# Kernel optimization log

Hardware: AMD Instinct MI355X
Metric: run time of the kernel (lower is better)

The kernel has to match this reference:

```python
import jax, jax.numpy as jnp
import numpy as np

N, S, E, HEADS = 8, 2048, 1024, 16


def setup_inputs() -> dict:
    root = jax.random.key(0)
    k1, k2, k3, k4, k5, k6 = jax.random.split(root, 6)
    query = jax.random.normal(k1, (N, S, E), jnp.float32)
    key_t = jax.random.normal(k2, (N, S, E), jnp.float32)
    value = jax.random.normal(k3, (N, S, E), jnp.float32)
    # mask broadcasts against the (buggy) energy tensor of shape (N, S, H, H)
    mask = jax.random.randint(k4, (1, 1, HEADS, HEADS), 0, 2, jnp.int32)
    # guarantee no all-masked softmax row (avoid NaN)
    diag = jnp.arange(HEADS)
    mask = mask.at[0, 0, diag, diag].set(1)
    W_out = jax.random.normal(k5, (E, E), jnp.float32) / np.float32(np.sqrt(E))
    b_out = jax.random.normal(k6, (E,), jnp.float32) * 0.02
    return {"query": query, "key": key_t, "value": value, "mask": mask,
            "W_out": W_out, "b_out": b_out, "heads": HEADS}


def reference(query, key, value, mask, W_out, b_out, heads):
    # Faithful translation of the original forward, INCLUDING its einsum-label
    # bug: tensors are transposed to (N, H, S, D) but the einsum subscripts
    # treat axis 1 as 'q/k' and axis 2 as 'h', so softmax runs over heads.
    n, q_len, e = query.shape
    d = e // heads
    inv_scale = np.float32(1.0 / np.sqrt(d))
    q = query.reshape(n, q_len, heads, d).transpose(0, 2, 1, 3)   # (N,H,S,D)
    k = key.reshape(n, q_len, heads, d).transpose(0, 2, 1, 3)     # (N,H,S,D)
    v = value.reshape(n, q_len, heads, d).transpose(0, 2, 1, 3)   # (N,H,S,D)
    # labels applied to transposed tensors -> energy shape (N, S, H, H)
    energy = jnp.einsum('nqhd,nkhd->nhqk', q, k) * inv_scale
    energy = jnp.where(mask == 0, -jnp.inf, energy)
    attention = jax.nn.softmax(energy, axis=-1)                   # over heads axis
    out = jnp.einsum('nhql,nlhd->nqhd', attention, v)             # (N,H,S,D)
    out = out.reshape(n, q_len, e)                                # raw memory reinterp, as torch does
    return out @ W_out.T + b_out
```

## Files before the change

### kernel.cpp

```cpp
#include <hip/hip_runtime.h>
#include <stdint.h>

#define S_LEN 2048
#define EMB 1024

typedef __bf16 bf16x8 __attribute__((ext_vector_type(8)));
typedef __bf16 bf16x4 __attribute__((ext_vector_type(4)));
typedef float f32x4 __attribute__((ext_vector_type(4)));

__device__ __forceinline__ unsigned short f2bf(float f) {
  unsigned int b = __float_as_uint(f);
  b += 0x7FFFu + ((b >> 16) & 1u);
  return (unsigned short)(b >> 16);
}

__device__ __forceinline__ bf16x8 cvt8(float4 a, float4 b) {
  bf16x8 r;
  r[0] = (__bf16)a.x; r[1] = (__bf16)a.y; r[2] = (__bf16)a.z; r[3] = (__bf16)a.w;
  r[4] = (__bf16)b.x; r[5] = (__bf16)b.y; r[6] = (__bf16)b.z; r[7] = (__bf16)b.w;
  return r;
}

#define GLD16(gp, lp)                                                          \
  __builtin_amdgcn_global_load_lds(                                            \
      (const __attribute__((address_space(1))) void*)(gp),                     \
      (__attribute__((address_space(3))) void*)(lp), 16, 0, 0)

__global__ __launch_bounds__(256) void attn_kernel(
    const float* __restrict__ Q, const float* __restrict__ K,
    const float* __restrict__ V, const int* __restrict__ mask,
    __bf16* __restrict__ X) {
  __shared__ __bf16 As[4][16][16];

  const int lane = threadIdx.x & 63;
  const int wv = threadIdx.x >> 6;
  const int pos = blockIdx.x * 4 + wv;
  const int n = pos >> 11;
  const int s = pos & 2047;
  const int col = lane & 15;
  const int grp = lane >> 4;
  const int gc = grp & 1;

  const float* qrow = Q + (size_t)pos * EMB;
  const float* krow = K + (size_t)pos * EMB;
  const float* vrow = V + (size_t)pos * EMB;

  const int fo = col * 64 + grp * 8;
  bf16x8 qa[2], kb[2];
#pragma unroll
  for (int t = 0; t < 2; ++t) {
    float4 a0 = *(const float4*)(qrow + fo + t * 32);
    float4 a1 = *(const float4*)(qrow + fo + t * 32 + 4);
    float4 b0 = *(const float4*)(krow + fo + t * 32);
    float4 b1 = *(const float4*)(krow + fo + t * 32 + 4);
    qa[t] = cvt8(a0, a1);
    kb[t] = cvt8(b0, b1);
  }

  f32x4 en = {0.f, 0.f, 0.f, 0.f};
  en = __builtin_amdgcn_mfma_f32_16x16x32_bf16(kb[0], qa[0], en, 0, 0, 0);
  en = __builtin_amdgcn_mfma_f32_16x16x32_bf16(kb[1], qa[1], en, 0, 0, 0);

  const int4 mrow = *(const int4*)(mask + col * 16 + grp * 4);
  float p[4];
  p[0] = (mrow.x == 0) ? -1e30f : en[0] * 0.125f;
  p[1] = (mrow.y == 0) ? -1e30f : en[1] * 0.125f;
  p[2] = (mrow.z == 0) ? -1e30f : en[2] * 0.125f;
  p[3] = (mrow.w == 0) ? -1e30f : en[3] * 0.125f;
  float mx = fmaxf(fmaxf(p[0], p[1]), fmaxf(p[2], p[3]));
  mx = fmaxf(mx, __shfl_xor(mx, 16));
  mx = fmaxf(mx, __shfl_xor(mx, 32));
  float ex[4], sm = 0.f;
#pragma unroll
  for (int r = 0; r < 4; ++r) {
    ex[r] = __expf(p[r] - mx);
    sm += ex[r];
  }
  sm += __shfl_xor(sm, 16);
  sm += __shfl_xor(sm, 32);
  const float inv = __builtin_amdgcn_rcpf(sm);

  bf16x4 aw;
#pragma unroll
  for (int r = 0; r < 4; ++r) aw[r] = (__bf16)(ex[r] * inv);
  *(bf16x4*)&As[wv][col][grp * 4] = aw;

  const bf16x8 pt = *(const bf16x8*)&As[wv][col][gc * 8];
  bf16x8 pa;
#pragma unroll
  for (int e = 0; e < 8; ++e) pa[e] = (grp < 2) ? pt[e] : (__bf16)0.f;

  const size_t xrow = (size_t)n * S_LEN + (size_t)col * 128 + (s >> 4);
  __bf16* xp = X + xrow * EMB + (size_t)((s & 15) * 64 + grp * 4);
#pragma unroll
  for (int c = 0; c < 4; ++c) {
    bf16x8 vf;
#pragma unroll
    for (int e = 0; e < 8; ++e)
      vf[e] = (__bf16)vrow[(gc * 8 + e) * 64 + c * 16 + col];
    f32x4 o = {0.f, 0.f, 0.f, 0.f};
    o = __builtin_amdgcn_mfma_f32_16x16x32_bf16(vf, pa, o, 0, 0, 0);
    bf16x4 w;
#pragma unroll
    for (int r = 0; r < 4; ++r) w[r] = (__bf16)o[r];
    *(bf16x4*)(xp + c * 16) = w;
  }
}

__global__ __launch_bounds__(256) void wconv_kernel(
    const float* __restrict__ W, unsigned short* __restrict__ Wb) {
  const int idx = blockIdx.x * 256 + threadIdx.x;
  float4 w = *(const float4*)(W + (size_t)idx * 4);
  ushort4 o;
  o.x = f2bf(w.x);
  o.y = f2bf(w.y);
  o.z = f2bf(w.z);
  o.w = f2bf(w.w);
  *(ushort4*)(Wb + (size_t)idx * 4) = o;
}

__global__ __launch_bounds__(256) void gemm_kernel(
    const unsigned short* __restrict__ A, const unsigned short* __restrict__ B,
    const float* __restrict__ bias, float* __restrict__ C) {
  __shared__ unsigned short sA[128 * 32];
  __shared__ unsigned short sB[128 * 32];

  int bid = blockIdx.x;
  const int cpx = gridDim.x >> 3;
  bid = (bid & 7) * cpx + (bid >> 3);
  const int tileM = (bid >> 3) * 128;
  const int tileN = (bid & 7) * 128;

  const int t = threadIdx.x;
  const int lane = t & 63;
  const int wid = t >> 6;
  const int wm = wid >> 1, wn = wid & 1;
  const int lrow = lane & 15;
  const int lgrp = lane >> 4;

  f32x4 acc[4][4];
#pragma unroll
  for (int a = 0; a < 4; ++a)
#pragma unroll
    for (int b = 0; b < 4; ++b) acc[a][b] = (f32x4){0.f, 0.f, 0.f, 0.f};

  const int row0 = t >> 2;
  const int kk = (t & 3) * 8;
  const size_t abase = ((size_t)(tileM + row0)) * 1024 + kk;
  const size_t bbase = ((size_t)(tileN + row0)) * 1024 + kk;

  for (int k0 = 0; k0 < 1024; k0 += 32) {
#pragma unroll
    for (int c = 0; c < 2; ++c) {
      GLD16(A + abase + (size_t)c * 64 * 1024 + k0,
            (char*)sA + c * 4096 + t * 16);
      GLD16(B + bbase + (size_t)c * 64 * 1024 + k0,
            (char*)sB + c * 4096 + t * 16);
    }
    __syncthreads();

    bf16x8 af[4], bfr[4];
#pragma unroll
    for (int mi = 0; mi < 4; ++mi)
      af[mi] = *(const bf16x8*)&sA[(wm * 64 + mi * 16 + lrow) * 32 + lgrp * 8];
#pragma unroll
    for (int ni = 0; ni < 4; ++ni)
      bfr[ni] = *(const bf16x8*)&sB[(wn * 64 + ni * 16 + lrow) * 32 + lgrp * 8];
#pragma unroll
    for (int mi = 0; mi < 4; ++mi)
#pragma unroll
      for (int ni = 0; ni < 4; ++ni)
        acc[mi][ni] = __builtin_amdgcn_mfma_f32_16x16x32_bf16(
            af[mi], bfr[ni], acc[mi][ni], 0, 0, 0);
    __syncthreads();
  }

#pragma unroll
  for (int ni = 0; ni < 4; ++ni) {
    const int colc = tileN + wn * 64 + ni * 16 + lrow;
    const float bv = bias[colc];
#pragma unroll
    for (int mi = 0; mi < 4; ++mi) {
      const int row = tileM + wm * 64 + mi * 16 + lgrp * 4;
#pragma unroll
      for (int r = 0; r < 4; ++r)
        C[(size_t)(row + r) * 1024 + colc] = acc[mi][ni][r] + bv;
    }
  }
}

extern "C" void kernel_launch(void* const* d_in, const int* in_sizes, int n_in,
                              void* d_out, int out_size, void* d_ws,
                              size_t ws_size, hipStream_t stream) {
  const float* Q = (const float*)d_in[0];
  const float* K = (const float*)d_in[1];
  const float* V = (const float*)d_in[2];
  const int* mask = (const int*)d_in[3];
  const float* W = (const float*)d_in[4];
  const float* bias = (const float*)d_in[5];
  float* out = (float*)d_out;

  __bf16* X = (__bf16*)d_ws;
  unsigned short* Wb =
      (unsigned short*)((char*)d_ws + (size_t)32 * 1024 * 1024);

  hipLaunchKernelGGL(attn_kernel, dim3(8 * S_LEN / 4), dim3(256), 0, stream, Q,
                     K, V, mask, X);
  hipLaunchKernelGGL(wconv_kernel, dim3(1024), dim3(256), 0, stream, W, Wb);
  hipLaunchKernelGGL(gemm_kernel, dim3(1024), dim3(256), 0, stream,
                     (const unsigned short*)X, Wb, bias, out);
}
```

Before: 100.7 us.

## Stage Q/K/V rows through LDS with swizzle and coalesce attention output stores

The attention kernel now loads each block's four Q, K and V rows into shared memory using direct global-to-LDS 16-byte loads, with an XOR swizzle on Q/K to avoid bank conflicts. Fragments are then read from LDS instead of through strided global gathers, especially for V, which was previously read element by element. Outputs are staged in an LDS buffer and written as contiguous 16-element bf16 vectors instead of scattered 4-element stores. This costs about 48KB of LDS per block plus extra barriers, which may limit occupancy.

```diff
diff --git a/kernel.cpp b/kernel.cpp
--- a/kernel.cpp
+++ b/kernel.cpp
@@ -26,42 +26,63 @@
       (const __attribute__((address_space(1))) void*)(gp),                     \
       (__attribute__((address_space(3))) void*)(lp), 16, 0, 0)
 
+__device__ __forceinline__ float4 lds_rd4(const float* base, int byteoff) {
+  const int sw = byteoff ^ (((byteoff >> 8) & 7) << 5);
+  return *(const float4*)((const char*)base + sw);
+}
+
 __global__ __launch_bounds__(256) void attn_kernel(
     const float* __restrict__ Q, const float* __restrict__ K,
     const float* __restrict__ V, const int* __restrict__ mask,
     __bf16* __restrict__ X) {
+  __shared__ float Qf[4][1024];
+  __shared__ float Kf[4][1024];
+  __shared__ float Vf[4][1024];
   __shared__ __bf16 As[4][16][16];
-
-  const int lane = threadIdx.x & 63;
-  const int wv = threadIdx.x >> 6;
-  const int pos = blockIdx.x * 4 + wv;
-  const int n = pos >> 11;
-  const int s = pos & 2047;
+  __shared__ __bf16 Ob[4][16][72];
+
+  const int t = threadIdx.x;
+  const int lane = t & 63;
+  const int wv = t >> 6;
+  const int pos0 = blockIdx.x * 4;
+  const int n = pos0 >> 11;
+  const int s0 = pos0 & 2047;
   const int col = lane & 15;
   const int grp = lane >> 4;
   const int gc = grp & 1;
 
-  const float* qrow = Q + (size_t)pos * EMB;
-  const float* krow = K + (size_t)pos * EMB;
-  const float* vrow = V + (size_t)pos * EMB;
-
-  const int fo = col * 64 + grp * 8;
-  bf16x8 qa[2], kb[2];
-#pragma unroll
-  for (int t = 0; t < 2; ++t) {
-    float4 a0 = *(const float4*)(qrow + fo + t * 32);
-    float4 a1 = *(const float4*)(qrow + fo + t * 32 + 4);
-    float4 b0 = *(const float4*)(krow + fo + t * 32);
-    float4 b1 = *(const float4*)(krow + fo + t * 32 + 4);
-    qa[t] = cvt8(a0, a1);
-    kb[t] = cvt8(b0, b1);
-  }
+  {
+    const int L = t * 16;
+    const int Lsw = L ^ (((L >> 8) & 7) << 5);
+#pragma unroll
+    for (int q = 0; q < 4; ++q) {
+      const char* qsrc = (const char*)(Q + (size_t)(pos0 + q) * EMB);
+      const char* ksrc = (const char*)(K + (size_t)(pos0 + q) * EMB);
+      const char* vsrc = (const char*)(V + (size_t)(pos0 + q) * EMB);
+      GLD16(qsrc + Lsw, (char*)&Qf[q][0] + L);
+      GLD16(ksrc + Lsw, (char*)&Kf[q][0] + L);
+      GLD16(vsrc + L, (char*)&Vf[q][0] + L);
+    }
+  }
+  const int4 mrow = *(const int4*)(mask + col * 16 + grp * 4);
+  __syncthreads();
+
+  const int R0 = col * 256 + grp * 32;
+  const float4 qA = lds_rd4(&Qf[wv][0], R0);
+  const float4 qB = lds_rd4(&Qf[wv][0], R0 + 16);
+  const float4 qC = lds_rd4(&Qf[wv][0], R0 + 128);
+  const float4 qD = lds_rd4(&Qf[wv][0], R0 + 144);
+  const float4 kA = lds_rd4(&Kf[wv][0], R0);
+  const float4 kB = lds_rd4(&Kf[wv][0], R0 + 16);
+  const float4 kC = lds_rd4(&Kf[wv][0], R0 + 128);
+  const float4 kD = lds_rd4(&Kf[wv][0], R0 + 144);
+  const bf16x8 qa0 = cvt8(qA, qB), qa1 = cvt8(qC, qD);
+  const bf16x8 kb0 = cvt8(kA, kB), kb1 = cvt8(kC, kD);
 
   f32x4 en = {0.f, 0.f, 0.f, 0.f};
-  en = __builtin_amdgcn_mfma_f32_16x16x32_bf16(kb[0], qa[0], en, 0, 0, 0);
-  en = __builtin_amdgcn_mfma_f32_16x16x32_bf16(kb[1], qa[1], en, 0, 0, 0);
-
-  const int4 mrow = *(const int4*)(mask + col * 16 + grp * 4);
+  en = __builtin_amdgcn_mfma_f32_16x16x32_bf16(kb0, qa0, en, 0, 0, 0);
+  en = __builtin_amdgcn_mfma_f32_16x16x32_bf16(kb1, qa1, en, 0, 0, 0);
+
   float p[4];
   p[0] = (mrow.x == 0) ? -1e30f : en[0] * 0.125f;
   p[1] = (mrow.y == 0) ? -1e30f : en[1] * 0.125f;
@@ -79,7 +100,6 @@
   sm += __shfl_xor(sm, 16);
   sm += __shfl_xor(sm, 32);
   const float inv = __builtin_amdgcn_rcpf(sm);
-
   bf16x4 aw;
 #pragma unroll
   for (int r = 0; r < 4; ++r) aw[r] = (__bf16)(ex[r] * inv);
@@ -90,20 +110,30 @@
 #pragma unroll
   for (int e = 0; e < 8; ++e) pa[e] = (grp < 2) ? pt[e] : (__bf16)0.f;
 
-  const size_t xrow = (size_t)n * S_LEN + (size_t)col * 128 + (s >> 4);
-  __bf16* xp = X + xrow * EMB + (size_t)((s & 15) * 64 + grp * 4);
 #pragma unroll
   for (int c = 0; c < 4; ++c) {
     bf16x8 vf;
 #pragma unroll
     for (int e = 0; e < 8; ++e)
-      vf[e] = (__bf16)vrow[(gc * 8 + e) * 64 + c * 16 + col];
+      vf[e] = (__bf16)Vf[wv][(gc * 8 + e) * 64 + c * 16 + col];
     f32x4 o = {0.f, 0.f, 0.f, 0.f};
     o = __builtin_amdgcn_mfma_f32_16x16x32_bf16(vf, pa, o, 0, 0, 0);
     bf16x4 w;
 #pragma unroll
     for (int r = 0; r < 4; ++r) w[r] = (__bf16)o[r];
-    *(bf16x4*)(xp + c * 16) = w;
+    *(bf16x4*)&Ob[wv][col][c * 16 + grp * 4] = w;
+  }
+  __syncthreads();
+
+  {
+    const int i = t >> 4;
+    const int o = (t & 15) * 16;
+    const int q = o >> 6;
+    const int d = o & 63;
+    const size_t row = (size_t)n * S_LEN + (size_t)i * 128 + (s0 >> 4);
+    __bf16* dst = &X[row * EMB + (size_t)((s0 & 15) * 64 + o)];
+    *(bf16x8*)dst = *(const bf16x8*)&Ob[q][i][d];
+    *(bf16x8*)(dst + 8) = *(const bf16x8*)&Ob[q][i][d + 8];
   }
 }
 
@@ -204,8 +234,8 @@
   unsigned short* Wb =
       (unsigned short*)((char*)d_ws + (size_t)32 * 1024 * 1024);
 
-  hipLaunchKernelGGL(attn_kernel, dim3(8 * S_LEN / 4), dim3(256), 0, stream, Q,
-                     K, V, mask, X);
+  hipLaunchKernelGGL(attn_kernel, dim3(8 * S_LEN / 4), dim3(256), 0, stream,
+                     Q, K, V, mask, X);
   hipLaunchKernelGGL(wconv_kernel, dim3(1024), dim3(256), 0, stream, W, Wb);
   hipLaunchKernelGGL(gemm_kernel, dim3(1024), dim3(256), 0, stream,
                      (const unsigned short*)X, Wb, bias, out);
```

After: 101.0 us. No clear change (+0.2%).

## Double-buffer Q/K/V rows into LDS via async loads in attention kernel

Applied to the files above, without the earlier changes.

Each attention block now processes 16 positions in 8 steps. Q, K and V rows are prefetched into swizzled LDS buffers with global_load_lds while the previous pair is computed. This aims for fully coalesced 16-byte loads and overlap of memory with the MFMA/softmax work. In exchange it uses 48KB of LDS per block and leaves half the waves idle during compute. It also launches a quarter as many blocks, which may reduce occupancy and latency hiding.

```diff
diff --git a/kernel.cpp b/kernel.cpp
--- a/kernel.cpp
+++ b/kernel.cpp
@@ -26,84 +26,116 @@
       (const __attribute__((address_space(1))) void*)(gp),                     \
       (__attribute__((address_space(3))) void*)(lp), 16, 0, 0)
 
+__device__ __forceinline__ float4 lds_rd4(const float* base, int byteoff) {
+  const int sw = byteoff ^ (((byteoff >> 8) & 7) << 5);
+  return *(const float4*)((const char*)base + sw);
+}
+
 __global__ __launch_bounds__(256) void attn_kernel(
     const float* __restrict__ Q, const float* __restrict__ K,
     const float* __restrict__ V, const int* __restrict__ mask,
     __bf16* __restrict__ X) {
-  __shared__ __bf16 As[4][16][16];
-
-  const int lane = threadIdx.x & 63;
-  const int wv = threadIdx.x >> 6;
-  const int pos = blockIdx.x * 4 + wv;
-  const int n = pos >> 11;
-  const int s = pos & 2047;
+  __shared__ float Qf[2][2][1024];
+  __shared__ float Kf[2][2][1024];
+  __shared__ float Vf[2][2][1024];
+  __shared__ __bf16 As[2][16][16];
+
+  const int t = threadIdx.x;
+  const int lane = t & 63;
+  const int wv = t >> 6;
+  const int pos0 = blockIdx.x * 16;
+  const int n = pos0 >> 11;
   const int col = lane & 15;
   const int grp = lane >> 4;
   const int gc = grp & 1;
 
-  const float* qrow = Q + (size_t)pos * EMB;
-  const float* krow = K + (size_t)pos * EMB;
-  const float* vrow = V + (size_t)pos * EMB;
-
-  const int fo = col * 64 + grp * 8;
-  bf16x8 qa[2], kb[2];
-#pragma unroll
-  for (int t = 0; t < 2; ++t) {
-    float4 a0 = *(const float4*)(qrow + fo + t * 32);
-    float4 a1 = *(const float4*)(qrow + fo + t * 32 + 4);
-    float4 b0 = *(const float4*)(krow + fo + t * 32);
-    float4 b1 = *(const float4*)(krow + fo + t * 32 + 4);
-    qa[t] = cvt8(a0, a1);
-    kb[t] = cvt8(b0, b1);
-  }
-
-  f32x4 en = {0.f, 0.f, 0.f, 0.f};
-  en = __builtin_amdgcn_mfma_f32_16x16x32_bf16(kb[0], qa[0], en, 0, 0, 0);
-  en = __builtin_amdgcn_mfma_f32_16x16x32_bf16(kb[1], qa[1], en, 0, 0, 0);
+  const int L = t * 16;
+  const int Lsw = L ^ (((L >> 8) & 7) << 5);
 
   const int4 mrow = *(const int4*)(mask + col * 16 + grp * 4);
-  float p[4];
-  p[0] = (mrow.x == 0) ? -1e30f : en[0] * 0.125f;
-  p[1] = (mrow.y == 0) ? -1e30f : en[1] * 0.125f;
-  p[2] = (mrow.z == 0) ? -1e30f : en[2] * 0.125f;
-  p[3] = (mrow.w == 0) ? -1e30f : en[3] * 0.125f;
-  float mx = fmaxf(fmaxf(p[0], p[1]), fmaxf(p[2], p[3]));
-  mx = fmaxf(mx, __shfl_xor(mx, 16));
-  mx = fmaxf(mx, __shfl_xor(mx, 32));
-  float ex[4], sm = 0.f;
-#pragma unroll
-  for (int r = 0; r < 4; ++r) {
-    ex[r] = __expf(p[r] - mx);
-    sm += ex[r];
-  }
-  sm += __shfl_xor(sm, 16);
-  sm += __shfl_xor(sm, 32);
-  const float inv = __builtin_amdgcn_rcpf(sm);
-
-  bf16x4 aw;
-#pragma unroll
-  for (int r = 0; r < 4; ++r) aw[r] = (__bf16)(ex[r] * inv);
-  *(bf16x4*)&As[wv][col][grp * 4] = aw;
-
-  const bf16x8 pt = *(const bf16x8*)&As[wv][col][gc * 8];
-  bf16x8 pa;
-#pragma unroll
-  for (int e = 0; e < 8; ++e) pa[e] = (grp < 2) ? pt[e] : (__bf16)0.f;
-
-  const size_t xrow = (size_t)n * S_LEN + (size_t)col * 128 + (s >> 4);
-  __bf16* xp = X + xrow * EMB + (size_t)((s & 15) * 64 + grp * 4);
-#pragma unroll
-  for (int c = 0; c < 4; ++c) {
-    bf16x8 vf;
-#pragma unroll
-    for (int e = 0; e < 8; ++e)
-      vf[e] = (__bf16)vrow[(gc * 8 + e) * 64 + c * 16 + col];
-    f32x4 o = {0.f, 0.f, 0.f, 0.f};
-    o = __builtin_amdgcn_mfma_f32_16x16x32_bf16(vf, pa, o, 0, 0, 0);
-    bf16x4 w;
-#pragma unroll
-    for (int r = 0; r < 4; ++r) w[r] = (__bf16)o[r];
-    *(bf16x4*)(xp + c * 16) = w;
+
+  auto STAGE = [&](int buf, int step) {
+#pragma unroll
+    for (int pp = 0; pp < 2; ++pp) {
+      const int pos = pos0 + step * 2 + pp;
+      const char* qsrc = (const char*)(Q + (size_t)pos * EMB);
+      const char* ksrc = (const char*)(K + (size_t)pos * EMB);
+      const char* vsrc = (const char*)(V + (size_t)pos * EMB);
+      GLD16(qsrc + Lsw, (char*)&Qf[buf][pp][0] + L);
+      GLD16(ksrc + Lsw, (char*)&Kf[buf][pp][0] + L);
+      GLD16(vsrc + L, (char*)&Vf[buf][pp][0] + L);
+    }
+  };
+
+  auto COMPUTE = [&](int buf, int step) {
+    if (wv >= 2) return;
+    const int pos = pos0 + step * 2 + wv;
+    const int s = pos & 2047;
+    const float* qf = &Qf[buf][wv][0];
+    const float* kf = &Kf[buf][wv][0];
+    const float* vf4 = &Vf[buf][wv][0];
+
+    const int R0 = col * 256 + grp * 32;
+    const bf16x8 qa0 = cvt8(lds_rd4(qf, R0), lds_rd4(qf, R0 + 16));
+    const bf16x8 qa1 = cvt8(lds_rd4(qf, R0 + 128), lds_rd4(qf, R0 + 144));
+    const bf16x8 kb0 = cvt8(lds_rd4(kf, R0), lds_rd4(kf, R0 + 16));
+    const bf16x8 kb1 = cvt8(lds_rd4(kf, R0 + 128), lds_rd4(kf, R0 + 144));
+
+    f32x4 en = {0.f, 0.f, 0.f, 0.f};
+    en = __builtin_amdgcn_mfma_f32_16x16x32_bf16(kb0, qa0, en, 0, 0, 0);
+    en = __builtin_amdgcn_mfma_f32_16x16x32_bf16(kb1, qa1, en, 0, 0, 0);
+
+    float p[4];
+    p[0] = (mrow.x == 0) ? -1e30f : en[0] * 0.125f;
+    p[1] = (mrow.y == 0) ? -1e30f : en[1] * 0.125f;
+    p[2] = (mrow.z == 0) ? -1e30f : en[2] * 0.125f;
+    p[3] = (mrow.w == 0) ? -1e30f : en[3] * 0.125f;
+    float mx = fmaxf(fmaxf(p[0], p[1]), fmaxf(p[2], p[3]));
+    mx = fmaxf(mx, __shfl_xor(mx, 16));
+    mx = fmaxf(mx, __shfl_xor(mx, 32));
+    float ex[4], sm = 0.f;
+#pragma unroll
+    for (int r = 0; r < 4; ++r) {
+      ex[r] = __expf(p[r] - mx);
+      sm += ex[r];
+    }
+    sm += __shfl_xor(sm, 16);
+    sm += __shfl_xor(sm, 32);
+    const float inv = __builtin_amdgcn_rcpf(sm);
+    bf16x4 aw;
+#pragma unroll
+    for (int r = 0; r < 4; ++r) aw[r] = (__bf16)(ex[r] * inv);
+    *(bf16x4*)&As[wv][col][grp * 4] = aw;
+
+    const bf16x8 pt = *(const bf16x8*)&As[wv][col][gc * 8];
+    bf16x8 pa;
+#pragma unroll
+    for (int e = 0; e < 8; ++e) pa[e] = (grp < 2) ? pt[e] : (__bf16)0.f;
+
+    const size_t xrow = (size_t)n * S_LEN + (size_t)col * 128 + (s >> 4);
+    __bf16* xp = X + xrow * EMB + (size_t)((s & 15) * 64 + grp * 4);
+#pragma unroll
+    for (int c = 0; c < 4; ++c) {
+      bf16x8 vf;
+#pragma unroll
+      for (int e = 0; e < 8; ++e)
+        vf[e] = (__bf16)vf4[(gc * 8 + e) * 64 + c * 16 + col];
+      f32x4 o = {0.f, 0.f, 0.f, 0.f};
+      o = __builtin_amdgcn_mfma_f32_16x16x32_bf16(vf, pa, o, 0, 0, 0);
+      bf16x4 w;
+#pragma unroll
+      for (int r = 0; r < 4; ++r) w[r] = (__bf16)o[r];
+      *(bf16x4*)(xp + c * 16) = w;
+    }
+  };
+
+  STAGE(0, 0);
+  __syncthreads();
+#pragma unroll 2
+  for (int step = 0; step < 8; ++step) {
+    if (step + 1 < 8) STAGE((step + 1) & 1, step + 1);
+    COMPUTE(step & 1, step);
+    __syncthreads();
   }
 }
 
@@ -204,8 +236,8 @@
   unsigned short* Wb =
       (unsigned short*)((char*)d_ws + (size_t)32 * 1024 * 1024);
 
-  hipLaunchKernelGGL(attn_kernel, dim3(8 * S_LEN / 4), dim3(256), 0, stream, Q,
-                     K, V, mask, X);
+  hipLaunchKernelGGL(attn_kernel, dim3(8 * S_LEN / 16), dim3(256), 0, stream,
+                     Q, K, V, mask, X);
   hipLaunchKernelGGL(wconv_kernel, dim3(1024), dim3(256), 0, stream, W, Wb);
   hipLaunchKernelGGL(gemm_kernel, dim3(1024), dim3(256), 0, stream,
                      (const unsigned short*)X, Wb, bias, out);
```

After: 107.0 us. 6.2% more time.
